# Performance work log

Measured on AMD Instinct MI355X. Metric: run time of the kernel, lower is better.

## Reference

```python
import jax, jax.numpy as jnp
import numpy as np

V, H, B, T = 100000, 512, 4096, 524288
EPS = 1e-5

def setup_inputs() -> dict:
    key = jax.random.key(0)
    ks = jax.random.split(key, 8)
    tokens = jax.random.randint(ks[0], (T,), 0, V, dtype=jnp.int32)
    seg_ids = jnp.sort(jax.random.randint(ks[1], (T,), 0, B, dtype=jnp.int32))
    t = jax.random.bernoulli(ks[2], 0.5, (B,)).astype(jnp.float32)
    emb = jax.random.normal(ks[3], (V, H), dtype=jnp.float32) * 0.1
    W1 = jax.random.normal(ks[4], (H, H), dtype=jnp.float32) * (1.0 / np.sqrt(H))
    b1 = jnp.zeros((H,), jnp.float32)
    gamma = jnp.ones((H,), jnp.float32)
    beta = jnp.zeros((H,), jnp.float32)
    w2 = jax.random.normal(ks[5], (H,), dtype=jnp.float32) * (1.0 / np.sqrt(H))
    b2 = jnp.zeros((), jnp.float32)
    return {"tokens": tokens, "seg_ids": seg_ids, "t": t, "emb": emb,
            "W1": W1, "b1": b1, "gamma": gamma, "beta": beta, "w2": w2, "b2": b2}

def reference(tokens, seg_ids, t, emb, W1, b1, gamma, beta, w2, b2):
    nb = t.shape[0]
    # fused gather + segment-mean (bag-of-words), replaces the per-sample loop
    gathered = emb[tokens]  # [T, H]
    sums = jax.ops.segment_sum(gathered, seg_ids, num_segments=nb)  # [B, H]
    counts = jax.ops.segment_sum(jnp.ones((tokens.shape[0],), jnp.float32), seg_ids, num_segments=nb)
    bow = sums / jnp.maximum(counts, 1.0)[:, None]  # [B, H]
    # Linear -> BatchNorm1d (training-mode batch stats, biased var) -> ReLU
    z = bow @ W1.T + b1  # [B, H]
    mu = jnp.mean(z, axis=0)
    var = jnp.mean((z - mu) ** 2, axis=0)
    zn = (z - mu) * jax.lax.rsqrt(var + EPS) * gamma + beta
    h = jax.nn.relu(zn)  # dropout treated as identity (eval mode) for determinism
    logits = h @ w2 + b2  # [B]
    # BCEWithLogitsLoss: mean(softplus(logit) - t*logit), numerically stable
    loss = jnp.mean(jnp.logaddexp(0.0, logits) - t * logits)
    return (loss, logits)
```

## Files before the change

kernel.cpp:

```cpp
#include <hip/hip_runtime.h>
#include <hip/hip_bf16.h>
#include <hip/hip_fp16.h>
#include <math.h>

constexpr int NTOK = 524288;
constexpr int NB   = 4096;
constexpr int H    = 512;
constexpr float EPS = 1e-5f;

typedef _Float16 half8 __attribute__((ext_vector_type(8)));
typedef float f32x4 __attribute__((ext_vector_type(4)));
typedef float fvec4 __attribute__((ext_vector_type(4)));
struct h4 { __half2 a, b; };

__global__ __launch_bounds__(256) void k_convert(
    const float* __restrict__ emb, h4* __restrict__ embh,
    const float* __restrict__ W1, h4* __restrict__ W1h) {
  const size_t bid = blockIdx.x;
  if (bid < 50000) {
    size_t i = bid * 256 + threadIdx.x;
    fvec4 v = __builtin_nontemporal_load((const fvec4*)emb + i);
    h4 o;
    o.a = __floats2half2_rn(v[0], v[1]);
    o.b = __floats2half2_rn(v[2], v[3]);
    embh[i] = o;
  } else {
    size_t i = (bid - 50000) * 256 + threadIdx.x;
    fvec4 v = *((const fvec4*)W1 + i);
    h4 o;
    o.a = __floats2half2_rn(v[0], v[1]);
    o.b = __floats2half2_rn(v[2], v[3]);
    W1h[i] = o;
  }
}

__global__ __launch_bounds__(256) void k_bounds(
    const int* __restrict__ seg, int* __restrict__ starts) {
  const int i = blockIdx.x * 256 + threadIdx.x;
  const int cur = seg[i];
  const int prev = (i == 0) ? -1 : seg[i - 1];
  for (int b = prev + 1; b <= cur; ++b) starts[b] = i;
  if (i == NTOK - 1) {
    for (int b = cur + 1; b <= NB; ++b) starts[b] = NTOK;
  }
}

__global__ __launch_bounds__(256) void k_gather_mean(
    const int* __restrict__ tokens, const int* __restrict__ starts,
    const half8* __restrict__ embh, half8* __restrict__ bow_h) {
  const int b = blockIdx.x;
  const int start = starts[b];
  const int end = starts[b + 1];

  const int tid = threadIdx.x;
  const int lane = tid & 63;
  const int g = tid >> 6;

  float acc[8] = {};
  int i = start + g;
  for (; i + 12 < end; i += 16) {
    half8 v0 = embh[(size_t)tokens[i]      * 64 + lane];
    half8 v1 = embh[(size_t)tokens[i + 4]  * 64 + lane];
    half8 v2 = embh[(size_t)tokens[i + 8]  * 64 + lane];
    half8 v3 = embh[(size_t)tokens[i + 12] * 64 + lane];
#pragma unroll
    for (int j = 0; j < 8; ++j)
      acc[j] += (float)v0[j] + (float)v1[j] + (float)v2[j] + (float)v3[j];
  }
  for (; i < end; i += 4) {
    half8 v0 = embh[(size_t)tokens[i] * 64 + lane];
#pragma unroll
    for (int j = 0; j < 8; ++j) acc[j] += (float)v0[j];
  }

  __shared__ float part[3][64][9];
  if (g > 0) {
#pragma unroll
    for (int j = 0; j < 8; ++j) part[g - 1][lane][j] = acc[j];
  }
  __syncthreads();
  if (g == 0) {
    const int cnt = end - start;
    const float s = 1.0f / (float)(cnt > 0 ? cnt : 1);
    half8 o;
#pragma unroll
    for (int j = 0; j < 8; ++j) {
      float v = acc[j] + part[0][lane][j] + part[1][lane][j] + part[2][lane][j];
      o[j] = (_Float16)(v * s);
    }
    bow_h[(size_t)b * 64 + lane] = o;
  }
}

__global__ __launch_bounds__(256) void k_gemm_mfma(
    const _Float16* __restrict__ A,
    const _Float16* __restrict__ Bw,
    const float* __restrict__ b1, float* __restrict__ C) {
  const int tid = threadIdx.x;
  const int lane = tid & 63;
  const int gw = blockIdx.x * 4 + (tid >> 6);
  const int m0 = (gw >> 3) * 16;
  const int n0 = (gw & 7) * 64;
  const int l15 = lane & 15, quad = lane >> 4;

  f32x4 acc0 = {}, acc1 = {}, acc2 = {}, acc3 = {};
  const _Float16* ap = A + (size_t)(m0 + l15) * H + quad * 8;
  const _Float16* bp = Bw + (size_t)(n0 + l15) * H + quad * 8;

#pragma unroll
  for (int k = 0; k < H; k += 32) {
    half8 af  = *(const half8*)(ap + k);
    half8 bf0 = *(const half8*)(bp + k);
    half8 bf1 = *(const half8*)(bp + 16 * H + k);
    half8 bf2 = *(const half8*)(bp + 32 * H + k);
    half8 bf3 = *(const half8*)(bp + 48 * H + k);
    acc0 = __builtin_amdgcn_mfma_f32_16x16x32_f16(af, bf0, acc0, 0, 0, 0);
    acc1 = __builtin_amdgcn_mfma_f32_16x16x32_f16(af, bf1, acc1, 0, 0, 0);
    acc2 = __builtin_amdgcn_mfma_f32_16x16x32_f16(af, bf2, acc2, 0, 0, 0);
    acc3 = __builtin_amdgcn_mfma_f32_16x16x32_f16(af, bf3, acc3, 0, 0, 0);
  }

  const float bn0v = b1[n0 + l15];
  const float bn1v = b1[n0 + 16 + l15];
  const float bn2v = b1[n0 + 32 + l15];
  const float bn3v = b1[n0 + 48 + l15];
  float* crow = C + (size_t)(m0 + quad * 4) * H + n0 + l15;
#pragma unroll
  for (int r = 0; r < 4; ++r) {
    crow[(size_t)r * H]      = acc0[r] + bn0v;
    crow[(size_t)r * H + 16] = acc1[r] + bn1v;
    crow[(size_t)r * H + 32] = acc2[r] + bn2v;
    crow[(size_t)r * H + 48] = acc3[r] + bn3v;
  }
}

__global__ __launch_bounds__(256) void k_colstats(
    const float* __restrict__ z, float* __restrict__ ps, float* __restrict__ pss) {
  const int blk = blockIdx.x;
  const int c0 = threadIdx.x * 2;
  const int r0 = blk * 16;
  float s0 = 0, s1 = 0, q0 = 0, q1 = 0;
#pragma unroll
  for (int r = 0; r < 16; ++r) {
    float2 v = *(const float2*)&z[(size_t)(r0 + r) * H + c0];
    s0 += v.x; s1 += v.y;
    q0 += v.x * v.x; q1 += v.y * v.y;
  }
  ps[blk * H + c0] = s0; ps[blk * H + c0 + 1] = s1;
  pss[blk * H + c0] = q0; pss[blk * H + c0 + 1] = q1;
}

__global__ __launch_bounds__(128) void k_finalize(
    const float* __restrict__ ps, const float* __restrict__ pss,
    const float* __restrict__ gamma, const float* __restrict__ beta,
    float* __restrict__ scale, float* __restrict__ shift,
    float* __restrict__ out) {
  const int c = blockIdx.x * 128 + threadIdx.x;
  if (c == 0) out[0] = 0.f;
  float s = 0, q = 0;
#pragma unroll 8
  for (int i = 0; i < 256; ++i) { s += ps[i * H + c]; q += pss[i * H + c]; }
  const float mu = s * (1.0f / NB);
  const float var = q * (1.0f / NB) - mu * mu;
  const float rstd = rsqrtf(var + EPS);
  const float sc = rstd * gamma[c];
  scale[c] = sc;
  shift[c] = beta[c] - mu * sc;
}

__global__ __launch_bounds__(256) void k_bn_dot(
    const float* __restrict__ z, const float* __restrict__ scale,
    const float* __restrict__ shift, const float* __restrict__ w2,
    const float* __restrict__ b2, const float* __restrict__ t,
    float* __restrict__ out) {
  const int tid = threadIdx.x;
  const int wave = tid >> 6, lane = tid & 63;
  const int b = blockIdx.x * 4 + wave;
  const float4* __restrict__ z4 = (const float4*)(z + (size_t)b * H);
  const float4* __restrict__ sc4 = (const float4*)scale;
  const float4* __restrict__ sh4 = (const float4*)shift;
  const float4* __restrict__ w24 = (const float4*)w2;
  float acc = 0.f;
#pragma unroll
  for (int i = lane; i < 128; i += 64) {
    float4 zv = z4[i], sc = sc4[i], sh = sh4[i], w = w24[i];
    float h0 = fmaxf(zv.x * sc.x + sh.x, 0.f);
    float h1 = fmaxf(zv.y * sc.y + sh.y, 0.f);
    float h2 = fmaxf(zv.z * sc.z + sh.z, 0.f);
    float h3 = fmaxf(zv.w * sc.w + sh.w, 0.f);
    acc += h0 * w.x + h1 * w.y + h2 * w.z + h3 * w.w;
  }
#pragma unroll
  for (int off = 32; off > 0; off >>= 1) acc += __shfl_down(acc, off, 64);

  __shared__ float ls[4];
  if (lane == 0) {
    const float logit = acc + b2[0];
    out[1 + b] = logit;
    const float sp = fmaxf(logit, 0.f) + log1pf(expf(-fabsf(logit)));
    ls[wave] = (sp - t[b] * logit) * (1.0f / NB);
  }
  __syncthreads();
  if (tid == 0) atomicAdd(out, ls[0] + ls[1] + ls[2] + ls[3]);
}

extern "C" void kernel_launch(void* const* d_in, const int* in_sizes, int n_in,
                              void* d_out, int out_size, void* d_ws, size_t ws_size,
                              hipStream_t stream) {
  const int*   tokens = (const int*)d_in[0];
  const int*   seg    = (const int*)d_in[1];
  const float* t      = (const float*)d_in[2];
  const float* emb    = (const float*)d_in[3];
  const float* W1     = (const float*)d_in[4];
  const float* b1     = (const float*)d_in[5];
  const float* gamma  = (const float*)d_in[6];
  const float* beta   = (const float*)d_in[7];
  const float* w2     = (const float*)d_in[8];
  const float* b2     = (const float*)d_in[9];
  float* out = (float*)d_out;

  char* wsb = (char*)d_ws;
  half8*    embh  = (half8*)wsb;
  _Float16* W1h   = (_Float16*)(wsb + 102400000);
  half8*    bow_h = (half8*)(wsb + 102924288);
  float*    z     = (float*)(wsb + 107118592);
  float*    ps    = (float*)(wsb + 115507200);
  float*    pss   = ps + 256 * H;
  float*    scale = pss + 256 * H;
  float*    shift = scale + H;
  int*      starts = (int*)(wsb + 116559872);

  k_convert<<<50256, 256, 0, stream>>>(emb, (h4*)embh, W1, (h4*)W1h);
  k_bounds<<<NTOK / 256, 256, 0, stream>>>(seg, starts);
  k_gather_mean<<<NB, 256, 0, stream>>>(tokens, starts, embh, bow_h);
  k_gemm_mfma<<<512, 256, 0, stream>>>((const _Float16*)bow_h, W1h, b1, z);
  k_colstats<<<256, 256, 0, stream>>>(z, ps, pss);
  k_finalize<<<4, 128, 0, stream>>>(ps, pss, gamma, beta, scale, shift, out);
  k_bn_dot<<<NB / 4, 256, 0, stream>>>(z, scale, shift, w2, b2, t, out);
}
```

Baseline: 428.3 us.

## Gather fp32 embeddings directly and fuse BN epilogue with grid barriers

Drops the per-call conversion of the whole embedding table to fp16. The gather now reads fp32 rows directly and converts only the bag means to fp16 for the GEMM. The W1 conversion and segment-bounds kernels merge into one prep kernel. Column stats, BN finalize and the BN/ReLU/dot/loss step become one kernel that uses atomic-counter grid barriers, which cuts launches and workspace traffic. In exchange the gather reads twice as many bytes per token, and the spin barriers assume all 256 blocks are resident at once.

After: 483.7 us. +12.9%, slower.

```diff
diff --git a/kernel.cpp b/kernel.cpp
--- a/kernel.cpp
+++ b/kernel.cpp
@@ -1,5 +1,4 @@
 #include <hip/hip_runtime.h>
-#include <hip/hip_bf16.h>
 #include <hip/hip_fp16.h>
 #include <math.h>
 
@@ -10,44 +9,36 @@
 
 typedef _Float16 half8 __attribute__((ext_vector_type(8)));
 typedef float f32x4 __attribute__((ext_vector_type(4)));
-typedef float fvec4 __attribute__((ext_vector_type(4)));
 struct h4 { __half2 a, b; };
 
-__global__ __launch_bounds__(256) void k_convert(
-    const float* __restrict__ emb, h4* __restrict__ embh,
-    const float* __restrict__ W1, h4* __restrict__ W1h) {
-  const size_t bid = blockIdx.x;
-  if (bid < 50000) {
-    size_t i = bid * 256 + threadIdx.x;
-    fvec4 v = __builtin_nontemporal_load((const fvec4*)emb + i);
-    h4 o;
-    o.a = __floats2half2_rn(v[0], v[1]);
-    o.b = __floats2half2_rn(v[2], v[3]);
-    embh[i] = o;
-  } else {
-    size_t i = (bid - 50000) * 256 + threadIdx.x;
-    fvec4 v = *((const fvec4*)W1 + i);
+__global__ __launch_bounds__(256) void k_prep(
+    const float* __restrict__ W1, h4* __restrict__ W1h,
+    const int* __restrict__ seg, int* __restrict__ starts,
+    unsigned* __restrict__ ctr, float* __restrict__ out) {
+  const int bid = blockIdx.x;
+  const int tid = threadIdx.x;
+  if (bid == 0 && tid < 2) { ctr[tid] = 0u; if (tid == 0) out[0] = 0.f; }
+  if (bid < 256) {
+    const int i = bid * 256 + tid;
+    f32x4 v = *((const f32x4*)W1 + i);
     h4 o;
     o.a = __floats2half2_rn(v[0], v[1]);
     o.b = __floats2half2_rn(v[2], v[3]);
     W1h[i] = o;
-  }
-}
-
-__global__ __launch_bounds__(256) void k_bounds(
-    const int* __restrict__ seg, int* __restrict__ starts) {
-  const int i = blockIdx.x * 256 + threadIdx.x;
-  const int cur = seg[i];
-  const int prev = (i == 0) ? -1 : seg[i - 1];
-  for (int b = prev + 1; b <= cur; ++b) starts[b] = i;
-  if (i == NTOK - 1) {
-    for (int b = cur + 1; b <= NB; ++b) starts[b] = NTOK;
+  } else {
+    const int i = (bid - 256) * 256 + tid;
+    const int cur = seg[i];
+    const int prev = (i == 0) ? -1 : seg[i - 1];
+    for (int b = prev + 1; b <= cur; ++b) starts[b] = i;
+    if (i == NTOK - 1) {
+      for (int b = cur + 1; b <= NB; ++b) starts[b] = NTOK;
+    }
   }
 }
 
 __global__ __launch_bounds__(256) void k_gather_mean(
     const int* __restrict__ tokens, const int* __restrict__ starts,
-    const half8* __restrict__ embh, half8* __restrict__ bow_h) {
+    const float* __restrict__ emb, h4* __restrict__ bow_h) {
   const int b = blockIdx.x;
   const int start = starts[b];
   const int end = starts[b + 1];
@@ -55,22 +46,30 @@
   const int tid = threadIdx.x;
   const int lane = tid & 63;
   const int g = tid >> 6;
+  const f32x4* e4 = (const f32x4*)emb;
 
   float acc[8] = {};
   int i = start + g;
   for (; i + 12 < end; i += 16) {
-    half8 v0 = embh[(size_t)tokens[i]      * 64 + lane];
-    half8 v1 = embh[(size_t)tokens[i + 4]  * 64 + lane];
-    half8 v2 = embh[(size_t)tokens[i + 8]  * 64 + lane];
-    half8 v3 = embh[(size_t)tokens[i + 12] * 64 + lane];
-#pragma unroll
-    for (int j = 0; j < 8; ++j)
-      acc[j] += (float)v0[j] + (float)v1[j] + (float)v2[j] + (float)v3[j];
+    const size_t r0 = (size_t)tokens[i]      * 128 + lane;
+    const size_t r1 = (size_t)tokens[i + 4]  * 128 + lane;
+    const size_t r2 = (size_t)tokens[i + 8]  * 128 + lane;
+    const size_t r3 = (size_t)tokens[i + 12] * 128 + lane;
+    f32x4 a0 = e4[r0], c0 = e4[r0 + 64];
+    f32x4 a1 = e4[r1], c1 = e4[r1 + 64];
+    f32x4 a2 = e4[r2], c2 = e4[r2 + 64];
+    f32x4 a3 = e4[r3], c3 = e4[r3 + 64];
+#pragma unroll
+    for (int j = 0; j < 4; ++j) {
+      acc[j]     += a0[j] + a1[j] + a2[j] + a3[j];
+      acc[4 + j] += c0[j] + c1[j] + c2[j] + c3[j];
+    }
   }
   for (; i < end; i += 4) {
-    half8 v0 = embh[(size_t)tokens[i] * 64 + lane];
-#pragma unroll
-    for (int j = 0; j < 8; ++j) acc[j] += (float)v0[j];
+    const size_t r0 = (size_t)tokens[i] * 128 + lane;
+    f32x4 a0 = e4[r0], c0 = e4[r0 + 64];
+#pragma unroll
+    for (int j = 0; j < 4; ++j) { acc[j] += a0[j]; acc[4 + j] += c0[j]; }
   }
 
   __shared__ float part[3][64][9];
@@ -82,13 +81,15 @@
   if (g == 0) {
     const int cnt = end - start;
     const float s = 1.0f / (float)(cnt > 0 ? cnt : 1);
-    half8 o;
-#pragma unroll
-    for (int j = 0; j < 8; ++j) {
-      float v = acc[j] + part[0][lane][j] + part[1][lane][j] + part[2][lane][j];
-      o[j] = (_Float16)(v * s);
-    }
-    bow_h[(size_t)b * 64 + lane] = o;
+    float v[8];
+#pragma unroll
+    for (int j = 0; j < 8; ++j)
+      v[j] = (acc[j] + part[0][lane][j] + part[1][lane][j] + part[2][lane][j]) * s;
+    h4 lo, hi;
+    lo.a = __floats2half2_rn(v[0], v[1]); lo.b = __floats2half2_rn(v[2], v[3]);
+    hi.a = __floats2half2_rn(v[4], v[5]); hi.b = __floats2half2_rn(v[6], v[7]);
+    bow_h[(size_t)b * 128 + lane]      = lo;
+    bow_h[(size_t)b * 128 + 64 + lane] = hi;
   }
 }
 
@@ -134,74 +135,112 @@
   }
 }
 
-__global__ __launch_bounds__(256) void k_colstats(
-    const float* __restrict__ z, float* __restrict__ ps, float* __restrict__ pss) {
-  const int blk = blockIdx.x;
-  const int c0 = threadIdx.x * 2;
-  const int r0 = blk * 16;
-  float s0 = 0, s1 = 0, q0 = 0, q1 = 0;
-#pragma unroll
-  for (int r = 0; r < 16; ++r) {
-    float2 v = *(const float2*)&z[(size_t)(r0 + r) * H + c0];
-    s0 += v.x; s1 += v.y;
-    q0 += v.x * v.x; q1 += v.y * v.y;
-  }
-  ps[blk * H + c0] = s0; ps[blk * H + c0 + 1] = s1;
-  pss[blk * H + c0] = q0; pss[blk * H + c0 + 1] = q1;
-}
-
-__global__ __launch_bounds__(128) void k_finalize(
-    const float* __restrict__ ps, const float* __restrict__ pss,
+__global__ __launch_bounds__(256) void k_epilogue(
+    const float* __restrict__ z,
     const float* __restrict__ gamma, const float* __restrict__ beta,
+    const float* __restrict__ w2, const float* __restrict__ b2,
+    const float* __restrict__ t,
+    float* __restrict__ ps, float* __restrict__ pss,
+    unsigned* __restrict__ ctr,
     float* __restrict__ scale, float* __restrict__ shift,
     float* __restrict__ out) {
-  const int c = blockIdx.x * 128 + threadIdx.x;
-  if (c == 0) out[0] = 0.f;
-  float s = 0, q = 0;
-#pragma unroll 8
-  for (int i = 0; i < 256; ++i) { s += ps[i * H + c]; q += pss[i * H + c]; }
-  const float mu = s * (1.0f / NB);
-  const float var = q * (1.0f / NB) - mu * mu;
-  const float rstd = rsqrtf(var + EPS);
-  const float sc = rstd * gamma[c];
-  scale[c] = sc;
-  shift[c] = beta[c] - mu * sc;
-}
-
-__global__ __launch_bounds__(256) void k_bn_dot(
-    const float* __restrict__ z, const float* __restrict__ scale,
-    const float* __restrict__ shift, const float* __restrict__ w2,
-    const float* __restrict__ b2, const float* __restrict__ t,
-    float* __restrict__ out) {
-  const int tid = threadIdx.x;
-  const int wave = tid >> 6, lane = tid & 63;
-  const int b = blockIdx.x * 4 + wave;
-  const float4* __restrict__ z4 = (const float4*)(z + (size_t)b * H);
-  const float4* __restrict__ sc4 = (const float4*)scale;
-  const float4* __restrict__ sh4 = (const float4*)shift;
-  const float4* __restrict__ w24 = (const float4*)w2;
-  float acc = 0.f;
-#pragma unroll
-  for (int i = lane; i < 128; i += 64) {
-    float4 zv = z4[i], sc = sc4[i], sh = sh4[i], w = w24[i];
-    float h0 = fmaxf(zv.x * sc.x + sh.x, 0.f);
-    float h1 = fmaxf(zv.y * sc.y + sh.y, 0.f);
-    float h2 = fmaxf(zv.z * sc.z + sh.z, 0.f);
-    float h3 = fmaxf(zv.w * sc.w + sh.w, 0.f);
-    acc += h0 * w.x + h1 * w.y + h2 * w.z + h3 * w.w;
-  }
-#pragma unroll
-  for (int off = 32; off > 0; off >>= 1) acc += __shfl_down(acc, off, 64);
-
-  __shared__ float ls[4];
-  if (lane == 0) {
-    const float logit = acc + b2[0];
-    out[1 + b] = logit;
-    const float sp = fmaxf(logit, 0.f) + log1pf(expf(-fabsf(logit)));
-    ls[wave] = (sp - t[b] * logit) * (1.0f / NB);
-  }
-  __syncthreads();
-  if (tid == 0) atomicAdd(out, ls[0] + ls[1] + ls[2] + ls[3]);
+  const int blk = blockIdx.x;
+  const int tid = threadIdx.x;
+  const int w = tid >> 6, lane = tid & 63;
+
+  {
+    const int c0 = tid * 2;
+    const int r0 = blk * 16;
+    float s0 = 0, s1 = 0, q0 = 0, q1 = 0;
+#pragma unroll
+    for (int r = 0; r < 16; ++r) {
+      float2 v = *(const float2*)&z[(size_t)(r0 + r) * H + c0];
+      s0 += v.x; s1 += v.y;
+      q0 += v.x * v.x; q1 += v.y * v.y;
+    }
+    ps[blk * H + c0] = s0;  ps[blk * H + c0 + 1] = s1;
+    pss[blk * H + c0] = q0; pss[blk * H + c0 + 1] = q1;
+  }
+  __threadfence();
+  __syncthreads();
+  if (tid == 0) {
+    __hip_atomic_fetch_add(ctr, 1u, __ATOMIC_ACQ_REL, __HIP_MEMORY_SCOPE_AGENT);
+    while (__hip_atomic_load(ctr, __ATOMIC_ACQUIRE, __HIP_MEMORY_SCOPE_AGENT) < 256u)
+      __builtin_amdgcn_s_sleep(8);
+  }
+  __syncthreads();
+
+  {
+    float2 pv = *(const float2*)&ps[(size_t)tid * H + 2 * blk];
+    float2 qv = *(const float2*)&pss[(size_t)tid * H + 2 * blk];
+    float v0 = pv.x, v1 = pv.y, v2 = qv.x, v3 = qv.y;
+#pragma unroll
+    for (int off = 32; off > 0; off >>= 1) {
+      v0 += __shfl_down(v0, off, 64); v1 += __shfl_down(v1, off, 64);
+      v2 += __shfl_down(v2, off, 64); v3 += __shfl_down(v3, off, 64);
+    }
+    __shared__ float red[4][4];
+    if (lane == 0) { red[w][0] = v0; red[w][1] = v1; red[w][2] = v2; red[w][3] = v3; }
+    __syncthreads();
+    if (tid == 0) {
+      const float s0 = red[0][0] + red[1][0] + red[2][0] + red[3][0];
+      const float s1 = red[0][1] + red[1][1] + red[2][1] + red[3][1];
+      const float q0 = red[0][2] + red[1][2] + red[2][2] + red[3][2];
+      const float q1 = red[0][3] + red[1][3] + red[2][3] + red[3][3];
+      const int c = 2 * blk;
+      const float mu0 = s0 * (1.0f / NB), mu1 = s1 * (1.0f / NB);
+      const float sc0 = rsqrtf(q0 * (1.0f / NB) - mu0 * mu0 + EPS) * gamma[c];
+      const float sc1 = rsqrtf(q1 * (1.0f / NB) - mu1 * mu1 + EPS) * gamma[c + 1];
+      scale[c] = sc0;     shift[c] = beta[c] - mu0 * sc0;
+      scale[c + 1] = sc1; shift[c + 1] = beta[c + 1] - mu1 * sc1;
+    }
+  }
+  __threadfence();
+  __syncthreads();
+  if (tid == 0) {
+    __hip_atomic_fetch_add(ctr + 1, 1u, __ATOMIC_ACQ_REL, __HIP_MEMORY_SCOPE_AGENT);
+    while (__hip_atomic_load(ctr + 1, __ATOMIC_ACQUIRE, __HIP_MEMORY_SCOPE_AGENT) < 256u)
+      __builtin_amdgcn_s_sleep(8);
+  }
+  __syncthreads();
+
+  {
+    __shared__ __align__(16) float sc_s[H], sh_s[H];
+    sc_s[tid] = scale[tid]; sc_s[256 + tid] = scale[256 + tid];
+    sh_s[tid] = shift[tid]; sh_s[256 + tid] = shift[256 + tid];
+    __syncthreads();
+    float lsum = 0.f;
+#pragma unroll
+    for (int rr = 0; rr < 4; ++rr) {
+      const int row = blk * 16 + w * 4 + rr;
+      const float4* z4 = (const float4*)(z + (size_t)row * H);
+      float acc = 0.f;
+#pragma unroll
+      for (int ii = 0; ii < 2; ++ii) {
+        const int idx = lane + ii * 64;
+        float4 zv = z4[idx];
+        float4 sc = *(const float4*)&sc_s[idx * 4];
+        float4 sh = *(const float4*)&sh_s[idx * 4];
+        float4 wv = ((const float4*)w2)[idx];
+        acc += fmaxf(zv.x * sc.x + sh.x, 0.f) * wv.x
+             + fmaxf(zv.y * sc.y + sh.y, 0.f) * wv.y
+             + fmaxf(zv.z * sc.z + sh.z, 0.f) * wv.z
+             + fmaxf(zv.w * sc.w + sh.w, 0.f) * wv.w;
+      }
+#pragma unroll
+      for (int off = 32; off > 0; off >>= 1) acc += __shfl_down(acc, off, 64);
+      if (lane == 0) {
+        const float logit = acc + b2[0];
+        out[1 + row] = logit;
+        const float sp = fmaxf(logit, 0.f) + log1pf(expf(-fabsf(logit)));
+        lsum += sp - t[row] * logit;
+      }
+    }
+    __shared__ float ls[4];
+    if (lane == 0) ls[w] = lsum;
+    __syncthreads();
+    if (tid == 0) atomicAdd(out, (ls[0] + ls[1] + ls[2] + ls[3]) * (1.0f / NB));
+  }
 }
 
 extern "C" void kernel_launch(void* const* d_in, const int* in_sizes, int n_in,
@@ -220,21 +259,19 @@
   float* out = (float*)d_out;
 
   char* wsb = (char*)d_ws;
-  half8*    embh  = (half8*)wsb;
-  _Float16* W1h   = (_Float16*)(wsb + 102400000);
-  half8*    bow_h = (half8*)(wsb + 102924288);
-  float*    z     = (float*)(wsb + 107118592);
-  float*    ps    = (float*)(wsb + 115507200);
+  _Float16* W1h   = (_Float16*)wsb;
+  h4*       bow_h = (h4*)(wsb + 524288);
+  float*    z     = (float*)(wsb + 4718592);
+  float*    ps    = (float*)(wsb + 13107200);
   float*    pss   = ps + 256 * H;
   float*    scale = pss + 256 * H;
   float*    shift = scale + H;
-  int*      starts = (int*)(wsb + 116559872);
-
-  k_convert<<<50256, 256, 0, stream>>>(emb, (h4*)embh, W1, (h4*)W1h);
-  k_bounds<<<NTOK / 256, 256, 0, stream>>>(seg, starts);
-  k_gather_mean<<<NB, 256, 0, stream>>>(tokens, starts, embh, bow_h);
+  int*      starts = (int*)(wsb + 14159872);
+  unsigned* ctr    = (unsigned*)(wsb + 14180352);
+
+  k_prep<<<2304, 256, 0, stream>>>(W1, (h4*)W1h, seg, starts, ctr, out);
+  k_gather_mean<<<NB, 256, 0, stream>>>(tokens, starts, emb, bow_h);
   k_gemm_mfma<<<512, 256, 0, stream>>>((const _Float16*)bow_h, W1h, b1, z);
-  k_colstats<<<256, 256, 0, stream>>>(z, ps, pss);
-  k_finalize<<<4, 128, 0, stream>>>(ps, pss, gamma, beta, scale, shift, out);
-  k_bn_dot<<<NB / 4, 256, 0, stream>>>(z, scale, shift, w2, b2, t, out);
-}
+  k_epilogue<<<256, 256, 0, stream>>>(z, gamma, beta, w2, b2, t,
+                                      ps, pss, ctr, scale, shift, out);
+}
```
